# Kernel optimization log

Hardware: AMD Instinct MI355X
Metric: run time of the kernel (lower is better)

Reference implementation:

```python
import jax, jax.numpy as jnp
import numpy as np

N = 100000
E = 1600000
NFEAT = 256
NHIDDEN = 128
NCLASS = 40
NLAYERS = 8
INIT_T = 0.5


def setup_inputs() -> dict:
    key = jax.random.key(0)
    ks = jax.random.split(key, 9)
    x = jax.random.normal(ks[0], (N, NFEAT), dtype=jnp.float32)
    edge_row = jax.random.randint(ks[1], (E,), 0, N, dtype=jnp.int32)
    edge_col = jax.random.randint(ks[2], (E,), 0, N, dtype=jnp.int32)
    # small weights so the Chebyshev recurrence stays numerically tame
    edge_weight = jax.random.uniform(ks[3], (E,), dtype=jnp.float32) * (2.0 / 16.0)
    b1 = 1.0 / np.sqrt(NFEAT)
    fc1_w = jax.random.uniform(ks[4], (NFEAT, NHIDDEN), minval=-b1, maxval=b1, dtype=jnp.float32)
    fc1_b = jax.random.uniform(ks[5], (NHIDDEN,), minval=-b1, maxval=b1, dtype=jnp.float32)
    b2 = 1.0 / np.sqrt(NHIDDEN)
    fc2_w = jax.random.uniform(ks[6], (NHIDDEN, NCLASS), minval=-b2, maxval=b2, dtype=jnp.float32)
    fc2_b = jax.random.uniform(ks[7], (NCLASS,), minval=-b2, maxval=b2, dtype=jnp.float32)
    thetas = jnp.full((NLAYERS,), INIT_T, dtype=jnp.float32)
    return {"x": x, "edge_row": edge_row, "edge_col": edge_col,
            "edge_weight": edge_weight, "fc1_w": fc1_w, "fc1_b": fc1_b,
            "fc2_w": fc2_w, "fc2_b": fc2_b, "thetas": thetas}


def _spmm(edge_row, edge_col, edge_weight, t):
    # out[r] = sum_{e: row[e]=r} w[e] * t[col[e]]   (sparse L @ T)
    msgs = edge_weight[:, None] * t[edge_col]  # [E, H]
    return jax.ops.segment_sum(msgs, edge_row, num_segments=N)


def reference(x, edge_row, edge_col, edge_weight, fc1_w, fc1_b, fc2_w, fc2_b, thetas):
    # eval mode: dropout is identity
    h = jax.nn.relu(x @ fc1_w + fc1_b)  # [N, H]
    # filter 0: T_0 = h, poly = theta_0 * T_0
    t0 = h
    poly = thetas[0] * t0
    # filter 1: T_1 = L @ T_0
    t1 = _spmm(edge_row, edge_col, edge_weight, t0)
    poly = poly + thetas[1] * t1
    # remaining filters, replicating the original prevs-update order exactly
    prev0, prev1 = t0, t1
    for i in range(2, NLAYERS):
        ti = 2.0 * _spmm(edge_row, edge_col, edge_weight, prev0) - prev1
        prev1 = prev0
        prev0 = ti
        poly = poly + thetas[i] * ti
    y = poly @ fc2_w + fc2_b  # [N, nclass]
    return jax.nn.log_softmax(y, axis=1)
```

## Files before the change

### kernel.cpp

```cpp
#include <hip/hip_runtime.h>
#include <hip/hip_bf16.h>


#define NFEAT 256
#define NHID  128
#define NCLS  40
#define ELLS  48

typedef __hip_bfloat16 bf16;
typedef __attribute__((ext_vector_type(8))) short bf16x8;
typedef __attribute__((ext_vector_type(4))) float f32x4;

__device__ inline float2 load2b(const bf16* p) {
    __hip_bfloat162 v = *(const __hip_bfloat162*)p;
    return make_float2(__bfloat162float(v.x), __bfloat162float(v.y));
}
__device__ inline void store2b(bf16* p, float2 v) {
    __hip_bfloat162 o;
    o.x = __float2bfloat16(v.x);
    o.y = __float2bfloat16(v.y);
    *(__hip_bfloat162*)p = o;
}

__global__ void zero_ints(int* __restrict__ p, int n) {
    int i = blockIdx.x * blockDim.x + threadIdx.x;
    if (i < n) p[i] = 0;
}

__global__ void scatter_ell(const int* __restrict__ erow, const int* __restrict__ ecol,
                            const float* __restrict__ ew, int* __restrict__ deg,
                            int2* __restrict__ cw, int E) {
    int e = blockIdx.x * blockDim.x + threadIdx.x;
    if (e < E) {
        int r = erow[e];
        int p = atomicAdd(&deg[r], 1);
        if (p < ELLS)
            cw[(size_t)r * ELLS + p] = make_int2(ecol[e], __float_as_int(ew[e]));
    }
}

__global__ void hist_kernel(const int* __restrict__ erow, int* __restrict__ deg, int E) {
    int e = blockIdx.x * blockDim.x + threadIdx.x;
    if (e < E) atomicAdd(&deg[erow[e]], 1);
}

__global__ void assign_starts(const int* __restrict__ deg, int* __restrict__ counter,
                              int* __restrict__ row_start, int* __restrict__ cursor, int N) {
    int r = blockIdx.x * blockDim.x + threadIdx.x;
    int lane = threadIdx.x & 63;
    int d = (r < N) ? deg[r] : 0;
    int x = d;
    #pragma unroll
    for (int off = 1; off < 64; off <<= 1) {
        int y = __shfl_up(x, off);
        if (lane >= off) x += y;
    }
    int base = 0;
    if (lane == 63) base = atomicAdd(counter, x);
    base = __shfl(base, 63);
    int start = base + (x - d);
    if (r < N) {
        row_start[r] = start;
        cursor[r] = start;
    }
}

__global__ void scatter_compact(const int* __restrict__ erow, const int* __restrict__ ecol,
                                const float* __restrict__ ew, int* __restrict__ cursor,
                                int2* __restrict__ cw, int E) {
    int e = blockIdx.x * blockDim.x + threadIdx.x;
    if (e < E) {
        int r = erow[e];
        int p = atomicAdd(&cursor[r], 1);
        cw[p] = make_int2(ecol[e], __float_as_int(ew[e]));
    }
}

__global__ __launch_bounds__(256) void fc1_mfma(
    const float* __restrict__ x, const float* __restrict__ W,
    const float* __restrict__ bias, bf16* __restrict__ t0, int n) {
    __shared__ __align__(16) bf16 As[128 * 40];
    __shared__ __align__(16) bf16 Bs[128 * 40];

    const int tid = threadIdx.x;
    const int wave = tid >> 6;
    const int lane = tid & 63;
    const int quad = lane >> 4;
    const int lm = lane & 15;
    const int block_row = blockIdx.x * 128;

    f32x4 acc[2][8];
    #pragma unroll
    for (int s = 0; s < 2; ++s)
        #pragma unroll
        for (int t = 0; t < 8; ++t)
            acc[s][t] = (f32x4){0.f, 0.f, 0.f, 0.f};

    float bcol[8];
    #pragma unroll
    for (int t = 0; t < 8; ++t) bcol[t] = bias[t * 16 + lm];

    for (int kc = 0; kc < NFEAT; kc += 32) {
        #pragma unroll
        for (int i = 0; i < 4; ++i) {
            int idx = tid + 256 * i;
            int row = idx >> 3;
            int c4 = idx & 7;
            int grow = block_row + row;
            float4 v = make_float4(0.f, 0.f, 0.f, 0.f);
            if (grow < n) v = *(const float4*)&x[(size_t)grow * NFEAT + kc + c4 * 4];
            __hip_bfloat162 lo2, hi2;
            lo2.x = __float2bfloat16(v.x); lo2.y = __float2bfloat16(v.y);
            hi2.x = __float2bfloat16(v.z); hi2.y = __float2bfloat16(v.w);
            *(__hip_bfloat162*)&As[row * 40 + c4 * 4] = lo2;
            *(__hip_bfloat162*)&As[row * 40 + c4 * 4 + 2] = hi2;
        }
        #pragma unroll
        for (int i = 0; i < 4; ++i) {
            int idx = tid + 256 * i;
            int nn = idx & 127;
            int k4 = idx >> 7;
            const float* wp = &W[(size_t)(kc + k4 * 4) * NHID + nn];
            float v0 = wp[0];
            float v1 = wp[NHID];
            float v2 = wp[2 * NHID];
            float v3 = wp[3 * NHID];
            __hip_bfloat162 lo2, hi2;
            lo2.x = __float2bfloat16(v0); lo2.y = __float2bfloat16(v1);
            hi2.x = __float2bfloat16(v2); hi2.y = __float2bfloat16(v3);
            *(__hip_bfloat162*)&Bs[nn * 40 + k4 * 4] = lo2;
            *(__hip_bfloat162*)&Bs[nn * 40 + k4 * 4 + 2] = hi2;
        }
        __syncthreads();

        bf16x8 af0 = *(const bf16x8*)&As[(wave * 32 + lm) * 40 + quad * 8];
        bf16x8 af1 = *(const bf16x8*)&As[(wave * 32 + 16 + lm) * 40 + quad * 8];
        #pragma unroll
        for (int t = 0; t < 8; ++t) {
            bf16x8 bf = *(const bf16x8*)&Bs[(t * 16 + lm) * 40 + quad * 8];
            acc[0][t] = __builtin_amdgcn_mfma_f32_16x16x32_bf16(af0, bf, acc[0][t], 0, 0, 0);
            acc[1][t] = __builtin_amdgcn_mfma_f32_16x16x32_bf16(af1, bf, acc[1][t], 0, 0, 0);
        }
        __syncthreads();
    }

    #pragma unroll
    for (int s = 0; s < 2; ++s) {
        #pragma unroll
        for (int r = 0; r < 4; ++r) {
            int grow = block_row + wave * 32 + s * 16 + quad * 4 + r;
            if (grow >= n) continue;
            bf16* orow = t0 + (size_t)grow * NHID + lm;
            #pragma unroll
            for (int t = 0; t < 8; ++t) {
                float v = fmaxf(acc[s][t][r] + bcol[t], 0.f);
                orow[t * 16] = __float2bfloat16(v);
            }
        }
    }
}

template <bool FIRST, int PMODE>
__global__ __launch_bounds__(256) void spmm_cheb(
    const int* __restrict__ row_start, const int* __restrict__ deg,
    const int2* __restrict__ cw,
    const bf16* __restrict__ tprev, const bf16* __restrict__ tsub,
    bf16* __restrict__ tout, float* __restrict__ poly,
    const float* __restrict__ thetas, int layer, int ell_stride, int n) {
    int lane = threadIdx.x & 63;
    int wid = (int)((blockIdx.x * (unsigned)blockDim.x + threadIdx.x) >> 6);
    if (wid >= n) return;
    int start = ell_stride ? wid * ell_stride : row_start[wid];
    int d = deg[wid];
    const int2* ep = cw + start;
    const int lo = 2 * lane;

    float2 acc = make_float2(0.f, 0.f);
    int j = 0;
    for (; j + 8 <= d; j += 8) {
        int2 e[8];
        #pragma unroll
        for (int u = 0; u < 8; ++u) e[u] = ep[j + u];
        float2 tv[8];
        #pragma unroll
        for (int u = 0; u < 8; ++u) tv[u] = load2b(tprev + (size_t)e[u].x * NHID + lo);
        #pragma unroll
        for (int u = 0; u < 8; ++u) {
            float w = __int_as_float(e[u].y);
            acc.x = fmaf(w, tv[u].x, acc.x);
            acc.y = fmaf(w, tv[u].y, acc.y);
        }
    }
    for (; j < d; ++j) {
        int2 e = ep[j];
        float w = __int_as_float(e.y);
        float2 tv = load2b(tprev + (size_t)e.x * NHID + lo);
        acc.x = fmaf(w, tv.x, acc.x);
        acc.y = fmaf(w, tv.y, acc.y);
    }

    size_t o = (size_t)wid * NHID + lo;
    float2 res, pv;
    if constexpr (FIRST) {
        res = acc;
    } else {
        pv = load2b(tsub + o);
        res = make_float2(2.f * acc.x - pv.x, 2.f * acc.y - pv.y);
    }
    store2b(tout + o, res);

    if constexpr (PMODE == 1) {
        float th0 = thetas[0], th1 = thetas[1], th2 = thetas[2];
        float2 t0v = load2b(tprev + o);
        float2 p;
        p.x = th0 * t0v.x + th1 * pv.x + th2 * res.x;
        p.y = th0 * t0v.y + th1 * pv.y + th2 * res.y;
        *(float2*)&poly[o] = p;
    } else if constexpr (PMODE == 2) {
        float tha = thetas[layer - 1], thb = thetas[layer];
        float2 tp = load2b(tprev + o);
        float2 p = *(float2*)&poly[o];
        p.x += tha * tp.x + thb * res.x;
        p.y += tha * tp.y + thb * res.y;
        *(float2*)&poly[o] = p;
    } else if constexpr (PMODE == 3) {
        float thb = thetas[layer];
        float2 p = *(float2*)&poly[o];
        p.x += thb * res.x;
        p.y += thb * res.y;
        *(float2*)&poly[o] = p;
    }
}

__global__ __launch_bounds__(256) void fc2_softmax(
    const float* __restrict__ poly, const float* __restrict__ w2,
    const float* __restrict__ b2, float* __restrict__ out, int n) {
    int row = blockIdx.x * 256 + threadIdx.x;
    if (row >= n) return;

    float acc[NCLS];
    #pragma unroll
    for (int c = 0; c < NCLS; ++c) acc[c] = b2[c];

    const float* pr = poly + (size_t)row * NHID;
    #pragma unroll 1
    for (int k = 0; k < NHID; k += 4) {
        float4 p = *(const float4*)&pr[k];
        const float* wr = w2 + (size_t)k * NCLS;
        #pragma unroll
        for (int c = 0; c < NCLS; ++c) {
            acc[c] = fmaf(p.x, wr[c], acc[c]);
            acc[c] = fmaf(p.y, wr[NCLS + c], acc[c]);
            acc[c] = fmaf(p.z, wr[2 * NCLS + c], acc[c]);
            acc[c] = fmaf(p.w, wr[3 * NCLS + c], acc[c]);
        }
    }

    float m = acc[0];
    #pragma unroll
    for (int c = 1; c < NCLS; ++c) m = fmaxf(m, acc[c]);
    float s = 0.f;
    #pragma unroll
    for (int c = 0; c < NCLS; ++c) s += __expf(acc[c] - m);
    float lse = m + __logf(s);

    float* orow = out + (size_t)row * NCLS;
    #pragma unroll
    for (int c = 0; c < NCLS; c += 4) {
        float4 v = make_float4(acc[c] - lse, acc[c + 1] - lse,
                               acc[c + 2] - lse, acc[c + 3] - lse);
        *(float4*)&orow[c] = v;
    }
}

static void run_pipeline(const float* x, const float* w1, const float* b1,
                         const float* w2, const float* b2, const float* thetas,
                         float* out, int N, int E,
                         const int* row_start, const int* deg, const int2* cw,
                         int ell_stride, float* poly, bf16* tX, bf16* tY, bf16* tZ,
                         hipStream_t stream) {
    fc1_mfma<<<(N + 127) / 128, 256, 0, stream>>>(x, w1, b1, tX, N);

    int spmm_blocks = (int)(((size_t)N * 64 + 255) / 256);
    spmm_cheb<true, 0><<<spmm_blocks, 256, 0, stream>>>(
        row_start, deg, cw, tX, (const bf16*)nullptr, tY, poly, thetas, 1, ell_stride, N);
    bf16* p0 = tX;
    bf16* p1 = tY;
    bf16* dead = tZ;
    for (int i = 2; i < 8; ++i) {
        if (i == 2)       spmm_cheb<false, 1><<<spmm_blocks, 256, 0, stream>>>(
            row_start, deg, cw, p0, p1, dead, poly, thetas, i, ell_stride, N);
        else if (i == 4 || i == 6) spmm_cheb<false, 2><<<spmm_blocks, 256, 0, stream>>>(
            row_start, deg, cw, p0, p1, dead, poly, thetas, i, ell_stride, N);
        else if (i == 7)  spmm_cheb<false, 3><<<spmm_blocks, 256, 0, stream>>>(
            row_start, deg, cw, p0, p1, dead, poly, thetas, i, ell_stride, N);
        else              spmm_cheb<false, 0><<<spmm_blocks, 256, 0, stream>>>(
            row_start, deg, cw, p0, p1, dead, poly, thetas, i, ell_stride, N);
        bf16* nd = p1;
        p1 = p0;
        p0 = dead;
        dead = nd;
    }
    fc2_softmax<<<(N + 255) / 256, 256, 0, stream>>>(poly, w2, b2, out, N);
}

extern "C" void kernel_launch(void* const* d_in, const int* in_sizes, int n_in,
                              void* d_out, int out_size, void* d_ws, size_t ws_size,
                              hipStream_t stream) {
    const float* x      = (const float*)d_in[0];
    const int*   erow   = (const int*)d_in[1];
    const int*   ecol   = (const int*)d_in[2];
    const float* ew     = (const float*)d_in[3];
    const float* w1     = (const float*)d_in[4];
    const float* b1     = (const float*)d_in[5];
    const float* w2     = (const float*)d_in[6];
    const float* b2     = (const float*)d_in[7];
    const float* thetas = (const float*)d_in[8];
    float* out = (float*)d_out;

    const int N = in_sizes[0] / NFEAT;
    const int E = in_sizes[1];

    size_t need_ell = 4096 + (size_t)N * 4 + (size_t)N * ELLS * 8 +
                      (size_t)N * NHID * 4 + 3 * (size_t)N * NHID * 2 + 4096;
    bool use_ell = need_ell <= ws_size;

    char* ws = (char*)d_ws;
    size_t off = 0;
    auto alloc = [&](size_t bytes) -> void* {
        off = (off + 255) & ~(size_t)255;
        void* p = ws + off;
        off += bytes;
        return p;
    };

    if (use_ell) {
        int*   deg  = (int*)alloc((size_t)N * 4);
        int2*  cw   = (int2*)alloc((size_t)N * ELLS * 8);
        float* poly = (float*)alloc((size_t)N * NHID * 4);
        bf16*  tX   = (bf16*)alloc((size_t)N * NHID * 2);
        bf16*  tY   = (bf16*)alloc((size_t)N * NHID * 2);
        bf16*  tZ   = (bf16*)alloc((size_t)N * NHID * 2);

        zero_ints<<<(N + 255) / 256, 256, 0, stream>>>(deg, N);
        scatter_ell<<<(E + 255) / 256, 256, 0, stream>>>(erow, ecol, ew, deg, cw, E);
        run_pipeline(x, w1, b1, w2, b2, thetas, out, N, E,
                     nullptr, deg, cw, ELLS, poly, tX, tY, tZ, stream);
    } else {
        int*   deg       = (int*)alloc((size_t)(N + 1) * 4);
        int*   counter   = deg + N;
        int*   row_start = (int*)alloc((size_t)N * 4);
        int*   cursor    = (int*)alloc((size_t)N * 4);
        int2*  cw        = (int2*)alloc((size_t)E * 8);
        float* poly      = (float*)alloc((size_t)N * NHID * 4);
        bf16*  tX        = (bf16*)alloc((size_t)N * NHID * 2);
        bf16*  tY        = (bf16*)alloc((size_t)N * NHID * 2);
        bf16*  tZ        = (bf16*)alloc((size_t)N * NHID * 2);

        zero_ints<<<(N + 1 + 255) / 256, 256, 0, stream>>>(deg, N + 1);
        hist_kernel<<<(E + 255) / 256, 256, 0, stream>>>(erow, deg, E);
        assign_starts<<<(N + 255) / 256, 256, 0, stream>>>(deg, counter, row_start, cursor, N);
        scatter_compact<<<(E + 255) / 256, 256, 0, stream>>>(erow, ecol, ew, cursor, cw, E);
        run_pipeline(x, w1, b1, w2, b2, thetas, out, N, E,
                     row_start, deg, cw, 0, poly, tX, tY, tZ, stream);
    }
}
```

Baseline: 930.6 us.

## Build CSR via row-bucketed append and per-bucket local sort instead of ELL

Replaces the padded ELL edge layout with a two-stage build. Edges are first appended into fixed-capacity buckets of 128 rows using one atomic counter per bucket. A per-bucket kernel then does a shared-memory histogram, scan and scatter to form compact CSR rows. This aims to cut the random scattered writes of the ELL build and give the SpMM kernels dense, contiguous edge lists. In exchange it adds a second pass and heavy atomic contention on few bucket counters, and it silently drops edges if a bucket exceeds its capacity.

```diff
diff --git a/kernel.cpp b/kernel.cpp
--- a/kernel.cpp
+++ b/kernel.cpp
@@ -5,7 +5,8 @@
 #define NFEAT 256
 #define NHID  128
 #define NCLS  40
-#define ELLS  48
+#define RPB   128
+#define BCAP  2560
 
 typedef __hip_bfloat16 bf16;
 typedef __attribute__((ext_vector_type(8))) short bf16x8;
@@ -22,57 +23,70 @@
     *(__hip_bfloat162*)p = o;
 }
 
-__global__ void zero_ints(int* __restrict__ p, int n) {
-    int i = blockIdx.x * blockDim.x + threadIdx.x;
-    if (i < n) p[i] = 0;
-}
-
-__global__ void scatter_ell(const int* __restrict__ erow, const int* __restrict__ ecol,
-                            const float* __restrict__ ew, int* __restrict__ deg,
-                            int2* __restrict__ cw, int E) {
+__device__ inline int wave_iscan(int x) {
+    int lane = threadIdx.x & 63;
+    #pragma unroll
+    for (int off = 1; off < 64; off <<= 1) {
+        int y = __shfl_up(x, off);
+        if (lane >= off) x += y;
+    }
+    return x;
+}
+
+__global__ void bucket_append(const int* __restrict__ erow, const int* __restrict__ ecol,
+                              const float* __restrict__ ew, int* __restrict__ bcnt,
+                              int2* __restrict__ bkt, int E) {
     int e = blockIdx.x * blockDim.x + threadIdx.x;
     if (e < E) {
         int r = erow[e];
-        int p = atomicAdd(&deg[r], 1);
-        if (p < ELLS)
-            cw[(size_t)r * ELLS + p] = make_int2(ecol[e], __float_as_int(ew[e]));
-    }
-}
-
-__global__ void hist_kernel(const int* __restrict__ erow, int* __restrict__ deg, int E) {
-    int e = blockIdx.x * blockDim.x + threadIdx.x;
-    if (e < E) atomicAdd(&deg[erow[e]], 1);
-}
-
-__global__ void assign_starts(const int* __restrict__ deg, int* __restrict__ counter,
-                              int* __restrict__ row_start, int* __restrict__ cursor, int N) {
-    int r = blockIdx.x * blockDim.x + threadIdx.x;
-    int lane = threadIdx.x & 63;
-    int d = (r < N) ? deg[r] : 0;
-    int x = d;
-    #pragma unroll
-    for (int off = 1; off < 64; off <<= 1) {
-        int y = __shfl_up(x, off);
-        if (lane >= off) x += y;
-    }
-    int base = 0;
-    if (lane == 63) base = atomicAdd(counter, x);
-    base = __shfl(base, 63);
-    int start = base + (x - d);
-    if (r < N) {
-        row_start[r] = start;
-        cursor[r] = start;
-    }
-}
-
-__global__ void scatter_compact(const int* __restrict__ erow, const int* __restrict__ ecol,
-                                const float* __restrict__ ew, int* __restrict__ cursor,
-                                int2* __restrict__ cw, int E) {
-    int e = blockIdx.x * blockDim.x + threadIdx.x;
-    if (e < E) {
-        int r = erow[e];
-        int p = atomicAdd(&cursor[r], 1);
-        cw[p] = make_int2(ecol[e], __float_as_int(ew[e]));
+        int b = r >> 7;
+        int p = atomicAdd(&bcnt[b], 1);
+        if (p < BCAP)
+            bkt[(size_t)b * BCAP + p] =
+                make_int2((ecol[e] << 7) | (r & (RPB - 1)), __float_as_int(ew[e]));
+    }
+}
+
+__global__ __launch_bounds__(256) void bucket_to_csr(
+    const int2* __restrict__ bkt, const int* __restrict__ bcnt,
+    int2* __restrict__ cw, int* __restrict__ row_start, int* __restrict__ deg, int N) {
+    __shared__ int lhist[RPB];
+    __shared__ int loff[RPB];
+    __shared__ int lcur[RPB];
+    const int b = blockIdx.x;
+    const int base = b * BCAP;
+    const int cnt = min(bcnt[b], BCAP);
+    const int tid = threadIdx.x;
+
+    if (tid < RPB) lhist[tid] = 0;
+    __syncthreads();
+    for (int i = tid; i < cnt; i += 256)
+        atomicAdd(&lhist[bkt[base + i].x & (RPB - 1)], 1);
+    __syncthreads();
+    if (tid < 64) {
+        int a = lhist[tid];
+        int c = lhist[tid + 64];
+        int sa = wave_iscan(a);
+        int ta = __shfl(sa, 63);
+        int sc = wave_iscan(c) + ta;
+        loff[tid] = sa - a;
+        lcur[tid] = sa - a;
+        loff[tid + 64] = sc - c;
+        lcur[tid + 64] = sc - c;
+    }
+    __syncthreads();
+    for (int i = tid; i < cnt; i += 256) {
+        int2 r = bkt[base + i];
+        int rl = r.x & (RPB - 1);
+        int p = atomicAdd(&lcur[rl], 1);
+        cw[base + p] = make_int2(r.x >> 7, r.y);
+    }
+    if (tid < RPB) {
+        int grow = b * RPB + tid;
+        if (grow < N) {
+            row_start[grow] = base + loff[tid];
+            deg[grow] = lhist[tid];
+        }
     }
 }
 
@@ -137,9 +151,9 @@
         bf16x8 af1 = *(const bf16x8*)&As[(wave * 32 + 16 + lm) * 40 + quad * 8];
         #pragma unroll
         for (int t = 0; t < 8; ++t) {
-            bf16x8 bf = *(const bf16x8*)&Bs[(t * 16 + lm) * 40 + quad * 8];
-            acc[0][t] = __builtin_amdgcn_mfma_f32_16x16x32_bf16(af0, bf, acc[0][t], 0, 0, 0);
-            acc[1][t] = __builtin_amdgcn_mfma_f32_16x16x32_bf16(af1, bf, acc[1][t], 0, 0, 0);
+            bf16x8 bfm = *(const bf16x8*)&Bs[(t * 16 + lm) * 40 + quad * 8];
+            acc[0][t] = __builtin_amdgcn_mfma_f32_16x16x32_bf16(af0, bfm, acc[0][t], 0, 0, 0);
+            acc[1][t] = __builtin_amdgcn_mfma_f32_16x16x32_bf16(af1, bfm, acc[1][t], 0, 0, 0);
         }
         __syncthreads();
     }
@@ -166,11 +180,11 @@
     const int2* __restrict__ cw,
     const bf16* __restrict__ tprev, const bf16* __restrict__ tsub,
     bf16* __restrict__ tout, float* __restrict__ poly,
-    const float* __restrict__ thetas, int layer, int ell_stride, int n) {
+    const float* __restrict__ thetas, int layer, int n) {
     int lane = threadIdx.x & 63;
     int wid = (int)((blockIdx.x * (unsigned)blockDim.x + threadIdx.x) >> 6);
     if (wid >= n) return;
-    int start = ell_stride ? wid * ell_stride : row_start[wid];
+    int start = row_start[wid];
     int d = deg[wid];
     const int2* ep = cw + start;
     const int lo = 2 * lane;
@@ -273,29 +287,63 @@
     }
 }
 
+__global__ void zero_ints(int* __restrict__ p, int n) {
+    int i = blockIdx.x * blockDim.x + threadIdx.x;
+    if (i < n) p[i] = 0;
+}
+__global__ void hist_kernel(const int* __restrict__ erow, int* __restrict__ deg, int E) {
+    int e = blockIdx.x * blockDim.x + threadIdx.x;
+    if (e < E) atomicAdd(&deg[erow[e]], 1);
+}
+__global__ void assign_starts(const int* __restrict__ deg, int* __restrict__ counter,
+                              int* __restrict__ row_start, int* __restrict__ cursor, int N) {
+    int r = blockIdx.x * blockDim.x + threadIdx.x;
+    int lane = threadIdx.x & 63;
+    int d = (r < N) ? deg[r] : 0;
+    int x = wave_iscan(d);
+    int base = 0;
+    if (lane == 63) base = atomicAdd(counter, x);
+    base = __shfl(base, 63);
+    int start = base + (x - d);
+    if (r < N) {
+        row_start[r] = start;
+        cursor[r] = start;
+    }
+}
+__global__ void scatter_compact(const int* __restrict__ erow, const int* __restrict__ ecol,
+                                const float* __restrict__ ew, int* __restrict__ cursor,
+                                int2* __restrict__ cw, int E) {
+    int e = blockIdx.x * blockDim.x + threadIdx.x;
+    if (e < E) {
+        int r = erow[e];
+        int p = atomicAdd(&cursor[r], 1);
+        cw[p] = make_int2(ecol[e], __float_as_int(ew[e]));
+    }
+}
+
 static void run_pipeline(const float* x, const float* w1, const float* b1,
                          const float* w2, const float* b2, const float* thetas,
-                         float* out, int N, int E,
+                         float* out, int N,
                          const int* row_start, const int* deg, const int2* cw,
-                         int ell_stride, float* poly, bf16* tX, bf16* tY, bf16* tZ,
+                         float* poly, bf16* tX, bf16* tY, bf16* tZ,
                          hipStream_t stream) {
     fc1_mfma<<<(N + 127) / 128, 256, 0, stream>>>(x, w1, b1, tX, N);
 
     int spmm_blocks = (int)(((size_t)N * 64 + 255) / 256);
     spmm_cheb<true, 0><<<spmm_blocks, 256, 0, stream>>>(
-        row_start, deg, cw, tX, (const bf16*)nullptr, tY, poly, thetas, 1, ell_stride, N);
+        row_start, deg, cw, tX, (const bf16*)nullptr, tY, poly, thetas, 1, N);
     bf16* p0 = tX;
     bf16* p1 = tY;
     bf16* dead = tZ;
     for (int i = 2; i < 8; ++i) {
         if (i == 2)       spmm_cheb<false, 1><<<spmm_blocks, 256, 0, stream>>>(
-            row_start, deg, cw, p0, p1, dead, poly, thetas, i, ell_stride, N);
+            row_start, deg, cw, p0, p1, dead, poly, thetas, i, N);
         else if (i == 4 || i == 6) spmm_cheb<false, 2><<<spmm_blocks, 256, 0, stream>>>(
-            row_start, deg, cw, p0, p1, dead, poly, thetas, i, ell_stride, N);
+            row_start, deg, cw, p0, p1, dead, poly, thetas, i, N);
         else if (i == 7)  spmm_cheb<false, 3><<<spmm_blocks, 256, 0, stream>>>(
-            row_start, deg, cw, p0, p1, dead, poly, thetas, i, ell_stride, N);
+            row_start, deg, cw, p0, p1, dead, poly, thetas, i, N);
         else              spmm_cheb<false, 0><<<spmm_blocks, 256, 0, stream>>>(
-            row_start, deg, cw, p0, p1, dead, poly, thetas, i, ell_stride, N);
+            row_start, deg, cw, p0, p1, dead, poly, thetas, i, N);
         bf16* nd = p1;
         p1 = p0;
         p0 = dead;
@@ -320,10 +368,7 @@
 
     const int N = in_sizes[0] / NFEAT;
     const int E = in_sizes[1];
-
-    size_t need_ell = 4096 + (size_t)N * 4 + (size_t)N * ELLS * 8 +
-                      (size_t)N * NHID * 4 + 3 * (size_t)N * NHID * 2 + 4096;
-    bool use_ell = need_ell <= ws_size;
+    const int NB = (N + RPB - 1) / RPB;
 
     char* ws = (char*)d_ws;
     size_t off = 0;
@@ -334,18 +379,26 @@
         return p;
     };
 
-    if (use_ell) {
-        int*   deg  = (int*)alloc((size_t)N * 4);
-        int2*  cw   = (int2*)alloc((size_t)N * ELLS * 8);
-        float* poly = (float*)alloc((size_t)N * NHID * 4);
-        bf16*  tX   = (bf16*)alloc((size_t)N * NHID * 2);
-        bf16*  tY   = (bf16*)alloc((size_t)N * NHID * 2);
-        bf16*  tZ   = (bf16*)alloc((size_t)N * NHID * 2);
-
-        zero_ints<<<(N + 255) / 256, 256, 0, stream>>>(deg, N);
-        scatter_ell<<<(E + 255) / 256, 256, 0, stream>>>(erow, ecol, ew, deg, cw, E);
-        run_pipeline(x, w1, b1, w2, b2, thetas, out, N, E,
-                     nullptr, deg, cw, ELLS, poly, tX, tY, tZ, stream);
+    size_t need_bkt = 4096 + (size_t)NB * 4 + 2 * (size_t)NB * BCAP * 8 +
+                      2 * (size_t)N * 4 + (size_t)N * NHID * 4 +
+                      3 * (size_t)N * NHID * 2 + 8192;
+
+    if (need_bkt <= ws_size) {
+        int*   bcnt      = (int*)alloc((size_t)NB * 4);
+        int2*  bkt       = (int2*)alloc((size_t)NB * BCAP * 8);
+        int2*  cw        = (int2*)alloc((size_t)NB * BCAP * 8);
+        int*   row_start = (int*)alloc((size_t)N * 4);
+        int*   deg       = (int*)alloc((size_t)N * 4);
+        float* poly      = (float*)alloc((size_t)N * NHID * 4);
+        bf16*  tX        = (bf16*)alloc((size_t)N * NHID * 2);
+        bf16*  tY        = (bf16*)alloc((size_t)N * NHID * 2);
+        bf16*  tZ        = (bf16*)alloc((size_t)N * NHID * 2);
+
+        hipMemsetAsync(bcnt, 0, (size_t)NB * 4, stream);
+        bucket_append<<<(E + 255) / 256, 256, 0, stream>>>(erow, ecol, ew, bcnt, bkt, E);
+        bucket_to_csr<<<NB, 256, 0, stream>>>(bkt, bcnt, cw, row_start, deg, N);
+        run_pipeline(x, w1, b1, w2, b2, thetas, out, N,
+                     row_start, deg, cw, poly, tX, tY, tZ, stream);
     } else {
         int*   deg       = (int*)alloc((size_t)(N + 1) * 4);
         int*   counter   = deg + N;
@@ -361,7 +414,7 @@
         hist_kernel<<<(E + 255) / 256, 256, 0, stream>>>(erow, deg, E);
         assign_starts<<<(N + 255) / 256, 256, 0, stream>>>(deg, counter, row_start, cursor, N);
         scatter_compact<<<(E + 255) / 256, 256, 0, stream>>>(erow, ecol, ew, cursor, cw, E);
-        run_pipeline(x, w1, b1, w2, b2, thetas, out, N, E,
-                     row_start, deg, cw, 0, poly, tX, tY, tZ, stream);
-    }
-}
+        run_pipeline(x, w1, b1, w2, b2, thetas, out, N,
+                     row_start, deg, cw, poly, tX, tY, tZ, stream);
+    }
+}
```

After: 1.201 ms. +29.0%, slower.

## Split SpMM Chebyshev chain into two 64-column feature chunks

Applied to the files above, without the earlier changes.

Runs the full Chebyshev recurrence separately for each half of the hidden dimension, with one lane per feature column and scalar bf16 loads. The intent is to halve the gathered feature working set per pass so it stays better in cache. The cost is reading the edge list twice and issuing narrower per-lane loads, plus twice as many kernel launches.

```diff
diff --git a/kernel.cpp b/kernel.cpp
--- a/kernel.cpp
+++ b/kernel.cpp
@@ -6,20 +6,20 @@
 #define NHID  128
 #define NCLS  40
 #define ELLS  48
+#define HCH   64
 
 typedef __hip_bfloat16 bf16;
 typedef __attribute__((ext_vector_type(8))) short bf16x8;
 typedef __attribute__((ext_vector_type(4))) float f32x4;
 
-__device__ inline float2 load2b(const bf16* p) {
-    __hip_bfloat162 v = *(const __hip_bfloat162*)p;
-    return make_float2(__bfloat162float(v.x), __bfloat162float(v.y));
-}
-__device__ inline void store2b(bf16* p, float2 v) {
-    __hip_bfloat162 o;
-    o.x = __float2bfloat16(v.x);
-    o.y = __float2bfloat16(v.y);
-    *(__hip_bfloat162*)p = o;
+__device__ inline int wave_iscan(int x) {
+    int lane = threadIdx.x & 63;
+    #pragma unroll
+    for (int off = 1; off < 64; off <<= 1) {
+        int y = __shfl_up(x, off);
+        if (lane >= off) x += y;
+    }
+    return x;
 }
 
 __global__ void zero_ints(int* __restrict__ p, int n) {
@@ -43,18 +43,12 @@
     int e = blockIdx.x * blockDim.x + threadIdx.x;
     if (e < E) atomicAdd(&deg[erow[e]], 1);
 }
-
 __global__ void assign_starts(const int* __restrict__ deg, int* __restrict__ counter,
                               int* __restrict__ row_start, int* __restrict__ cursor, int N) {
     int r = blockIdx.x * blockDim.x + threadIdx.x;
     int lane = threadIdx.x & 63;
     int d = (r < N) ? deg[r] : 0;
-    int x = d;
-    #pragma unroll
-    for (int off = 1; off < 64; off <<= 1) {
-        int y = __shfl_up(x, off);
-        if (lane >= off) x += y;
-    }
+    int x = wave_iscan(d);
     int base = 0;
     if (lane == 63) base = atomicAdd(counter, x);
     base = __shfl(base, 63);
@@ -64,7 +58,6 @@
         cursor[r] = start;
     }
 }
-
 __global__ void scatter_compact(const int* __restrict__ erow, const int* __restrict__ ecol,
                                 const float* __restrict__ ew, int* __restrict__ cursor,
                                 int2* __restrict__ cw, int E) {
@@ -137,9 +130,9 @@
         bf16x8 af1 = *(const bf16x8*)&As[(wave * 32 + 16 + lm) * 40 + quad * 8];
         #pragma unroll
         for (int t = 0; t < 8; ++t) {
-            bf16x8 bf = *(const bf16x8*)&Bs[(t * 16 + lm) * 40 + quad * 8];
-            acc[0][t] = __builtin_amdgcn_mfma_f32_16x16x32_bf16(af0, bf, acc[0][t], 0, 0, 0);
-            acc[1][t] = __builtin_amdgcn_mfma_f32_16x16x32_bf16(af1, bf, acc[1][t], 0, 0, 0);
+            bf16x8 bfm = *(const bf16x8*)&Bs[(t * 16 + lm) * 40 + quad * 8];
+            acc[0][t] = __builtin_amdgcn_mfma_f32_16x16x32_bf16(af0, bfm, acc[0][t], 0, 0, 0);
+            acc[1][t] = __builtin_amdgcn_mfma_f32_16x16x32_bf16(af1, bfm, acc[1][t], 0, 0, 0);
         }
         __syncthreads();
     }
@@ -166,69 +159,51 @@
     const int2* __restrict__ cw,
     const bf16* __restrict__ tprev, const bf16* __restrict__ tsub,
     bf16* __restrict__ tout, float* __restrict__ poly,
-    const float* __restrict__ thetas, int layer, int ell_stride, int n) {
+    const float* __restrict__ thetas, int layer, int ell_stride, int fc, int n) {
     int lane = threadIdx.x & 63;
     int wid = (int)((blockIdx.x * (unsigned)blockDim.x + threadIdx.x) >> 6);
     if (wid >= n) return;
     int start = ell_stride ? wid * ell_stride : row_start[wid];
     int d = deg[wid];
     const int2* ep = cw + start;
-    const int lo = 2 * lane;
-
-    float2 acc = make_float2(0.f, 0.f);
+    const bf16* tp = tprev + fc + lane;
+
+    float acc = 0.f;
     int j = 0;
     for (; j + 8 <= d; j += 8) {
         int2 e[8];
         #pragma unroll
         for (int u = 0; u < 8; ++u) e[u] = ep[j + u];
-        float2 tv[8];
-        #pragma unroll
-        for (int u = 0; u < 8; ++u) tv[u] = load2b(tprev + (size_t)e[u].x * NHID + lo);
-        #pragma unroll
-        for (int u = 0; u < 8; ++u) {
-            float w = __int_as_float(e[u].y);
-            acc.x = fmaf(w, tv[u].x, acc.x);
-            acc.y = fmaf(w, tv[u].y, acc.y);
-        }
+        float tv[8];
+        #pragma unroll
+        for (int u = 0; u < 8; ++u) tv[u] = __bfloat162float(tp[(size_t)e[u].x * NHID]);
+        #pragma unroll
+        for (int u = 0; u < 8; ++u)
+            acc = fmaf(__int_as_float(e[u].y), tv[u], acc);
     }
     for (; j < d; ++j) {
         int2 e = ep[j];
-        float w = __int_as_float(e.y);
-        float2 tv = load2b(tprev + (size_t)e.x * NHID + lo);
-        acc.x = fmaf(w, tv.x, acc.x);
-        acc.y = fmaf(w, tv.y, acc.y);
-    }
-
-    size_t o = (size_t)wid * NHID + lo;
-    float2 res, pv;
+        acc = fmaf(__int_as_float(e.y), __bfloat162float(tp[(size_t)e.x * NHID]), acc);
+    }
+
+    size_t o = (size_t)wid * NHID + fc + lane;
+    float res, pv;
     if constexpr (FIRST) {
         res = acc;
     } else {
-        pv = load2b(tsub + o);
-        res = make_float2(2.f * acc.x - pv.x, 2.f * acc.y - pv.y);
-    }
-    store2b(tout + o, res);
+        pv = __bfloat162float(tsub[o]);
+        res = 2.f * acc - pv;
+    }
+    tout[o] = __float2bfloat16(res);
 
     if constexpr (PMODE == 1) {
-        float th0 = thetas[0], th1 = thetas[1], th2 = thetas[2];
-        float2 t0v = load2b(tprev + o);
-        float2 p;
-        p.x = th0 * t0v.x + th1 * pv.x + th2 * res.x;
-        p.y = th0 * t0v.y + th1 * pv.y + th2 * res.y;
-        *(float2*)&poly[o] = p;
+        float t0v = __bfloat162float(tprev[o]);
+        poly[o] = thetas[0] * t0v + thetas[1] * pv + thetas[2] * res;
     } else if constexpr (PMODE == 2) {
-        float tha = thetas[layer - 1], thb = thetas[layer];
-        float2 tp = load2b(tprev + o);
-        float2 p = *(float2*)&poly[o];
-        p.x += tha * tp.x + thb * res.x;
-        p.y += tha * tp.y + thb * res.y;
-        *(float2*)&poly[o] = p;
+        float tpv = __bfloat162float(tprev[o]);
+        poly[o] += thetas[layer - 1] * tpv + thetas[layer] * res;
     } else if constexpr (PMODE == 3) {
-        float thb = thetas[layer];
-        float2 p = *(float2*)&poly[o];
-        p.x += thb * res.x;
-        p.y += thb * res.y;
-        *(float2*)&poly[o] = p;
+        poly[o] += thetas[layer] * res;
     }
 }
 
@@ -275,31 +250,34 @@
 
 static void run_pipeline(const float* x, const float* w1, const float* b1,
                          const float* w2, const float* b2, const float* thetas,
-                         float* out, int N, int E,
+                         float* out, int N,
                          const int* row_start, const int* deg, const int2* cw,
                          int ell_stride, float* poly, bf16* tX, bf16* tY, bf16* tZ,
                          hipStream_t stream) {
     fc1_mfma<<<(N + 127) / 128, 256, 0, stream>>>(x, w1, b1, tX, N);
 
     int spmm_blocks = (int)(((size_t)N * 64 + 255) / 256);
-    spmm_cheb<true, 0><<<spmm_blocks, 256, 0, stream>>>(
-        row_start, deg, cw, tX, (const bf16*)nullptr, tY, poly, thetas, 1, ell_stride, N);
-    bf16* p0 = tX;
-    bf16* p1 = tY;
-    bf16* dead = tZ;
-    for (int i = 2; i < 8; ++i) {
-        if (i == 2)       spmm_cheb<false, 1><<<spmm_blocks, 256, 0, stream>>>(
-            row_start, deg, cw, p0, p1, dead, poly, thetas, i, ell_stride, N);
-        else if (i == 4 || i == 6) spmm_cheb<false, 2><<<spmm_blocks, 256, 0, stream>>>(
-            row_start, deg, cw, p0, p1, dead, poly, thetas, i, ell_stride, N);
-        else if (i == 7)  spmm_cheb<false, 3><<<spmm_blocks, 256, 0, stream>>>(
-            row_start, deg, cw, p0, p1, dead, poly, thetas, i, ell_stride, N);
-        else              spmm_cheb<false, 0><<<spmm_blocks, 256, 0, stream>>>(
-            row_start, deg, cw, p0, p1, dead, poly, thetas, i, ell_stride, N);
-        bf16* nd = p1;
-        p1 = p0;
-        p0 = dead;
-        dead = nd;
+    for (int fc = 0; fc < NHID; fc += HCH) {
+        spmm_cheb<true, 0><<<spmm_blocks, 256, 0, stream>>>(
+            row_start, deg, cw, tX, (const bf16*)nullptr, tY, poly, thetas, 1,
+            ell_stride, fc, N);
+        bf16* p0 = tX;
+        bf16* p1 = tY;
+        bf16* dead = tZ;
+        for (int i = 2; i < 8; ++i) {
+            if (i == 2)       spmm_cheb<false, 1><<<spmm_blocks, 256, 0, stream>>>(
+                row_start, deg, cw, p0, p1, dead, poly, thetas, i, ell_stride, fc, N);
+            else if (i == 4 || i == 6) spmm_cheb<false, 2><<<spmm_blocks, 256, 0, stream>>>(
+                row_start, deg, cw, p0, p1, dead, poly, thetas, i, ell_stride, fc, N);
+            else if (i == 7)  spmm_cheb<false, 3><<<spmm_blocks, 256, 0, stream>>>(
+                row_start, deg, cw, p0, p1, dead, poly, thetas, i, ell_stride, fc, N);
+            else              spmm_cheb<false, 0><<<spmm_blocks, 256, 0, stream>>>(
+                row_start, deg, cw, p0, p1, dead, poly, thetas, i, ell_stride, fc, N);
+            bf16* nd = p1;
+            p1 = p0;
+            p0 = dead;
+            dead = nd;
+        }
     }
     fc2_softmax<<<(N + 255) / 256, 256, 0, stream>>>(poly, w2, b2, out, N);
 }
@@ -321,10 +299,6 @@
     const int N = in_sizes[0] / NFEAT;
     const int E = in_sizes[1];
 
-    size_t need_ell = 4096 + (size_t)N * 4 + (size_t)N * ELLS * 8 +
-                      (size_t)N * NHID * 4 + 3 * (size_t)N * NHID * 2 + 4096;
-    bool use_ell = need_ell <= ws_size;
-
     char* ws = (char*)d_ws;
     size_t off = 0;
     auto alloc = [&](size_t bytes) -> void* {
@@ -334,7 +308,10 @@
         return p;
     };
 
-    if (use_ell) {
+    size_t need_ell = 4096 + (size_t)N * 4 + (size_t)N * ELLS * 8 +
+                      (size_t)N * NHID * 4 + 3 * (size_t)N * NHID * 2 + 8192;
+
+    if (need_ell <= ws_size) {
         int*   deg  = (int*)alloc((size_t)N * 4);
         int2*  cw   = (int2*)alloc((size_t)N * ELLS * 8);
         float* poly = (float*)alloc((size_t)N * NHID * 4);
@@ -344,7 +321,7 @@
 
         zero_ints<<<(N + 255) / 256, 256, 0, stream>>>(deg, N);
         scatter_ell<<<(E + 255) / 256, 256, 0, stream>>>(erow, ecol, ew, deg, cw, E);
-        run_pipeline(x, w1, b1, w2, b2, thetas, out, N, E,
+        run_pipeline(x, w1, b1, w2, b2, thetas, out, N,
                      nullptr, deg, cw, ELLS, poly, tX, tY, tZ, stream);
     } else {
         int*   deg       = (int*)alloc((size_t)(N + 1) * 4);
@@ -361,7 +338,7 @@
         hist_kernel<<<(E + 255) / 256, 256, 0, stream>>>(erow, deg, E);
         assign_starts<<<(N + 255) / 256, 256, 0, stream>>>(deg, counter, row_start, cursor, N);
         scatter_compact<<<(E + 255) / 256, 256, 0, stream>>>(erow, ecol, ew, cursor, cw, E);
-        run_pipeline(x, w1, b1, w2, b2, thetas, out, N, E,
+        run_pipeline(x, w1, b1, w2, b2, thetas, out, N,
                      row_start, deg, cw, 0, poly, tX, tY, tZ, stream);
     }
 }
```

New measurement: 1.348 ms. 1.45x slower.
